# Optimization experiments

Hardware: AMD Instinct MI355X
Metric: run time of the kernel (lower is better)

Reference implementation:

```python
import jax, jax.numpy as jnp
import numpy as np

HEADS = 8
DIM_HEAD = 64
SPARSITY = 0.1  # sparsity_target * min(1, step_count/1000) with step_count >= 1000


def setup_inputs() -> dict:
    key = jax.random.key(0)
    k1, k2, k3, k4, k5 = jax.random.split(key, 5)
    b, n, d = 4, 2048, 512
    inner = HEADS * DIM_HEAD  # 512
    x = jax.random.normal(k1, (b, n, d), dtype=jnp.float32)
    # grad_ema buffer: EMA of squared attention gradients -> positive values
    grad_ema = jax.random.uniform(k2, (b, HEADS, n, n), dtype=jnp.float32)
    w_qkv = jax.random.normal(k3, (d, 3 * inner), dtype=jnp.float32) * 0.02
    w_out = jax.random.normal(k4, (inner, d), dtype=jnp.float32) * 0.02
    b_out = jax.random.normal(k5, (d,), dtype=jnp.float32) * 0.02
    return {"x": x, "grad_ema": grad_ema, "w_qkv": w_qkv, "w_out": w_out, "b_out": b_out}


def reference(x, grad_ema, w_qkv, w_out, b_out):
    b, n, d = x.shape
    h, dh = HEADS, DIM_HEAD
    scale = dh ** (-0.5)
    # QKV projection (no bias)
    qkv = x @ w_qkv  # [b, n, 3*h*dh]
    q, k, v = jnp.split(qkv, 3, axis=-1)
    def heads(t):  # [b, n, h*dh] -> [b, h, n, dh]
        return t.reshape(b, n, h, dh).transpose(0, 2, 1, 3)
    q, k, v = heads(q), heads(k), heads(v)
    dots = jnp.einsum("bhid,bhjd->bhij", q, k) * scale  # [b, h, n, n]
    # gradient-sculpted sparsity mask: keep entries with grad_ema above global quantile
    threshold = jnp.quantile(grad_ema, 1.0 - SPARSITY)
    dots = jnp.where(grad_ema >= threshold, dots, -jnp.inf)
    attn = jax.nn.softmax(dots, axis=-1)
    out = jnp.einsum("bhij,bhjd->bhid", attn, v)  # [b, h, n, dh]
    out = out.transpose(0, 2, 1, 3).reshape(b, n, h * dh)
    return out @ w_out + b_out
```

## Files before the change

kernel.cpp:

```cpp
#include <hip/hip_runtime.h>

typedef unsigned short u16;
typedef unsigned long long ull;
typedef __attribute__((ext_vector_type(8))) short bf16x8;
typedef __attribute__((ext_vector_type(4))) float f32x4;

#define LOG2E 1.44269504088896340736f

#define GN 134217728LL
#define LO_BITS 0x3F65FD8Bu
#define HI_BITS 0x3F66CF41u
#define NBINS (HI_BITS - LO_BITS)
#define SCAN_CHUNK 1024
#define NCHUNK ((int)((NBINS + SCAN_CHUNK - 1) / SCAN_CHUNK))

__device__ inline u16 f2bf(float f) {
    unsigned int u = __float_as_uint(f);
    unsigned int r = 0x7FFFu + ((u >> 16) & 1u);
    return (u16)((u + r) >> 16);
}

extern "C" __global__ __launch_bounds__(256)
void zero_k(unsigned int* __restrict__ hist, ull* __restrict__ hi_cnt) {
    int i = blockIdx.x * 256 + threadIdx.x;
    for (int b = i; b < (int)NBINS; b += 65536) hist[b] = 0u;
    if (i == 0) *hi_cnt = 0ull;
}

extern "C" __global__ __launch_bounds__(256)
void hist_k(const float* __restrict__ g, unsigned int* __restrict__ hist,
            ull* __restrict__ hi_cnt) {
    long long tid = (long long)blockIdx.x * 256 + threadIdx.x;
    long long stride = (long long)gridDim.x * 256;
    unsigned int hi = 0;
    const float4* g4 = (const float4*)g;
    const long long n4 = GN / 4;
    for (long long i = tid; i < n4; i += stride) {
        float4 v = g4[i];
        float vv[4] = {v.x, v.y, v.z, v.w};
#pragma unroll
        for (int c = 0; c < 4; ++c) {
            unsigned int u = __float_as_uint(vv[c]);
            if (u >= HI_BITS) hi++;
            else if (u >= LO_BITS) atomicAdd(&hist[u - LO_BITS], 1u);
        }
    }
#pragma unroll
    for (int off = 32; off; off >>= 1) hi += __shfl_down(hi, off, 64);
    if ((threadIdx.x & 63) == 0 && hi) atomicAdd(hi_cnt, (ull)hi);
}

extern "C" __global__ __launch_bounds__(256)
void scan_a(const unsigned int* __restrict__ hist, ull* __restrict__ csum) {
    __shared__ unsigned int part[256];
    int c = blockIdx.x;
    unsigned int s = 0;
    int base = c * SCAN_CHUNK;
    for (int i = threadIdx.x; i < SCAN_CHUNK; i += 256) {
        int b = base + i;
        if (b < (int)NBINS) s += hist[b];
    }
    part[threadIdx.x] = s;
    __syncthreads();
    for (int st = 128; st; st >>= 1) {
        if ((int)threadIdx.x < st) part[threadIdx.x] += part[threadIdx.x + st];
        __syncthreads();
    }
    if (threadIdx.x == 0) csum[c] = part[0];
}

extern "C" __global__ __launch_bounds__(256)
void scan_b(const unsigned int* __restrict__ hist, const ull* __restrict__ csum,
            const ull* __restrict__ hi_cnt, float* __restrict__ thr_out) {
    __shared__ ull cs[NCHUNK];
    __shared__ ull pre[NCHUNK];
    __shared__ ull cfine_s;
    __shared__ unsigned int wtot[4];
    __shared__ int ch_s;
    __shared__ ull chpre_s;
    __shared__ float vals_s[2];
    const int t = threadIdx.x;
    if (t < NCHUNK) cs[t] = csum[t];
    __syncthreads();
    if (t < NCHUNK) {
        ull s = 0;
        for (int j = 0; j < t; ++j) s += cs[j];
        pre[t] = s;
    }
    if (t == 0) {
        ull s = 0;
        for (int j = 0; j < NCHUNK; ++j) s += cs[j];
        cfine_s = s;
    }
    __syncthreads();
    const long long cfine = (long long)cfine_s;
    const long long chi = (long long)(*hi_cnt);
    const long long cbelow = GN - chi - cfine;
    const double h = 0.9 * (double)(GN - 1);
    const long long k = (long long)h;
    const double gfrac = h - (double)k;
    const long long tg0 = k - cbelow;

    for (int ti = 0; ti < 2; ++ti) {
        long long tgt = tg0 + ti;
        if (tgt < 0) { if (t == 0) vals_s[ti] = __uint_as_float(LO_BITS); __syncthreads(); continue; }
        if (tgt >= cfine) { if (t == 0) vals_s[ti] = __uint_as_float(HI_BITS); __syncthreads(); continue; }
        if (t < NCHUNK) {
            ull p = pre[t];
            if ((ull)tgt >= p && (ull)tgt < p + cs[t]) { ch_s = t; chpre_s = p; }
        }
        __syncthreads();
        const int base = ch_s * SCAN_CHUNK;
        const long long rel = tgt - (long long)chpre_s;
        unsigned int h4[4], s4 = 0;
#pragma unroll
        for (int q = 0; q < 4; ++q) {
            int b = base + t * 4 + q;
            unsigned int v = (b < (int)NBINS) ? hist[b] : 0u;
            h4[q] = v; s4 += v;
        }
        unsigned int sc = s4;
#pragma unroll
        for (int off = 1; off < 64; off <<= 1) {
            unsigned int y = __shfl_up(sc, off, 64);
            if ((t & 63) >= off) sc += y;
        }
        if ((t & 63) == 63) wtot[t >> 6] = sc;
        __syncthreads();
        unsigned int wbase = 0;
        for (int wv = 0; wv < (t >> 6); ++wv) wbase += wtot[wv];
        unsigned int incl = sc + wbase;
        unsigned int excl = incl - s4;
        if (rel >= (long long)excl && rel < (long long)incl) {
            long long rr = rel - excl;
            long long c2 = 0;
            int bsel = 3;
#pragma unroll
            for (int q = 0; q < 4; ++q) {
                if (c2 + (long long)h4[q] > rr) { bsel = q; break; }
                c2 += h4[q];
            }
            vals_s[ti] = __uint_as_float(LO_BITS + (unsigned int)(base + t * 4 + bsel));
        }
        __syncthreads();
    }
    if (t == 0) {
        double tv = (double)vals_s[0] + gfrac * ((double)vals_s[1] - (double)vals_s[0]);
        float tf = (float)tv;
        if ((double)tf < tv) tf = __uint_as_float(__float_as_uint(tf) + 1u);
        *thr_out = tf;
    }
}

extern "C" __global__ __launch_bounds__(256)
void conv_wt2(const float* __restrict__ wqkv, const float* __restrict__ wout,
              u16* __restrict__ wqt, u16* __restrict__ wot) {
    int bid = blockIdx.x;
    const float* w; u16* wt; int N; int id;
    if (bid < 3072) { w = wqkv; wt = wqt; N = 1536; id = bid * 256 + threadIdx.x; }
    else { w = wout; wt = wot; N = 512; id = (bid - 3072) * 256 + threadIdx.x; }
    int c = id / 512, k = id % 512;
    wt[id] = f2bf(w[(size_t)k * N + c]);
}

template <int MODE>
__global__ __launch_bounds__(256)
void gemm_bt(const float* __restrict__ Af, const u16* __restrict__ Ab, const u16* __restrict__ Bt,
             int M, int N, int K,
             u16* __restrict__ Qo, u16* __restrict__ Ko, u16* __restrict__ Vt,
             float* __restrict__ Cout, const float* __restrict__ bias) {
    __shared__ __align__(16) u16 As[128][64];
    __shared__ __align__(16) u16 Bs[128][64];
    const int t = threadIdx.x, w = t >> 6, l = t & 63;
    const int bm = blockIdx.x * 128, bn = blockIdx.y * 128;
    const int wm = (w >> 1) * 64, wn = (w & 1) * 64;
    const int lr = l & 15, lg = l >> 4;
    f32x4 acc[4][4] = {};
    for (int k0 = 0; k0 < K; k0 += 64) {
#pragma unroll
        for (int it = 0; it < 4; ++it) {
            int idx = it * 256 + t;
            int row = idx >> 3, ch = idx & 7;
            if constexpr (MODE == 0) {
                const float4* ap = (const float4*)&Af[(size_t)(bm + row) * K + k0 + ch * 8];
                float4 a0 = ap[0], a1 = ap[1];
                u16 tmp[8] = {f2bf(a0.x), f2bf(a0.y), f2bf(a0.z), f2bf(a0.w),
                              f2bf(a1.x), f2bf(a1.y), f2bf(a1.z), f2bf(a1.w)};
                *(bf16x8*)&As[row][(ch ^ (row & 7)) * 8] = *(bf16x8*)tmp;
            } else {
                *(bf16x8*)&As[row][(ch ^ (row & 7)) * 8] =
                    *(const bf16x8*)&Ab[(size_t)(bm + row) * K + k0 + ch * 8];
            }
        }
#pragma unroll
        for (int it = 0; it < 4; ++it) {
            int idx = it * 256 + t;
            int row = idx >> 3, ch = idx & 7;
            *(bf16x8*)&Bs[row][(ch ^ (row & 7)) * 8] =
                *(const bf16x8*)&Bt[(size_t)(bn + row) * K + k0 + ch * 8];
        }
        __syncthreads();
#pragma unroll
        for (int ks = 0; ks < 2; ++ks) {
            bf16x8 af[4], bfr[4];
#pragma unroll
            for (int i = 0; i < 4; ++i) {
                int row = wm + i * 16 + lr;
                int ci = ks * 4 + lg;
                af[i] = *(const bf16x8*)&As[row][(ci ^ (row & 7)) * 8];
            }
#pragma unroll
            for (int j = 0; j < 4; ++j) {
                int row = wn + j * 16 + lr;
                int ci = ks * 4 + lg;
                bfr[j] = *(const bf16x8*)&Bs[row][(ci ^ (row & 7)) * 8];
            }
#pragma unroll
            for (int i = 0; i < 4; ++i)
#pragma unroll
                for (int j = 0; j < 4; ++j)
                    acc[i][j] = __builtin_amdgcn_mfma_f32_16x16x32_bf16(af[i], bfr[j], acc[i][j], 0, 0, 0);
        }
        __syncthreads();
    }
#pragma unroll
    for (int i = 0; i < 4; ++i) {
#pragma unroll
        for (int j = 0; j < 4; ++j) {
            int col = bn + wn + j * 16 + lr;
#pragma unroll
            for (int r = 0; r < 4; ++r) {
                int row = bm + wm + i * 16 + lg * 4 + r;
                float v = acc[i][j][r];
                if constexpr (MODE == 0) {
                    int t3 = col >> 9;
                    int hh = (col >> 6) & 7;
                    int d = col & 63;
                    int b = row >> 11;
                    int tok = row & 2047;
                    int bh = b * 8 + hh;
                    if (t3 == 0) Qo[((size_t)bh * 2048 + tok) * 64 + d] = f2bf(v * 0.125f);
                    else if (t3 == 1) Ko[((size_t)bh * 2048 + tok) * 64 + d] = f2bf(v);
                    else Vt[((size_t)bh * 64 + d) * 2048 + tok] = f2bf(v);
                } else {
                    Cout[(size_t)row * N + col] = v + bias[col];
                }
            }
        }
    }
}

extern "C" __global__ __launch_bounds__(256)
void flash_k(const u16* __restrict__ Qb, const u16* __restrict__ Kb, const u16* __restrict__ Vt,
             const float* __restrict__ gema, const float* __restrict__ thrp,
             u16* __restrict__ HO) {
    __shared__ __align__(16) u16 Ks[64][64];
    __shared__ __align__(16) u16 Vs[64][64];
    __shared__ __align__(16) u16 Ps[4][32][64];
    const int t = threadIdx.x, w = t >> 6, l = t & 63;
    const int lr = l & 15, lg = l >> 4;
    const int bh = blockIdx.y;
    const int i0 = blockIdx.x * 128 + w * 32;
    const float thr = thrp[0];

    bf16x8 qf[2][2];
#pragma unroll
    for (int i2 = 0; i2 < 2; ++i2)
#pragma unroll
        for (int ks = 0; ks < 2; ++ks)
            qf[i2][ks] = *(const bf16x8*)&Qb[((size_t)bh * 2048 + i0 + i2 * 16 + lr) * 64 + ks * 32 + lg * 8];

    f32x4 o[2][4] = {};
    float mrow[2][4], lrow[2][4];
#pragma unroll
    for (int i2 = 0; i2 < 2; ++i2)
#pragma unroll
        for (int r = 0; r < 4; ++r) { mrow[i2][r] = -1e30f; lrow[i2][r] = 0.f; }

    const size_t gbase = (size_t)bh * 2048 * 2048;

    for (int jt = 0; jt < 2048; jt += 64) {
#pragma unroll
        for (int it = 0; it < 2; ++it) {
            int idx = it * 256 + t;
            int row = idx >> 3, ch = idx & 7;
            *(bf16x8*)&Ks[row][(ch ^ (row & 7)) * 8] =
                *(const bf16x8*)&Kb[((size_t)bh * 2048 + jt + row) * 64 + ch * 8];
            *(bf16x8*)&Vs[row][(ch ^ (row & 7)) * 8] =
                *(const bf16x8*)&Vt[((size_t)bh * 64 + row) * 2048 + jt + ch * 8];
        }
        __syncthreads();

        f32x4 sc[2][4] = {};
#pragma unroll
        for (int ks = 0; ks < 2; ++ks) {
#pragma unroll
            for (int jf = 0; jf < 4; ++jf) {
                int row = jf * 16 + lr;
                int ci = ks * 4 + lg;
                bf16x8 kf = *(const bf16x8*)&Ks[row][(ci ^ (row & 7)) * 8];
#pragma unroll
                for (int i2 = 0; i2 < 2; ++i2)
                    sc[i2][jf] = __builtin_amdgcn_mfma_f32_16x16x32_bf16(qf[i2][ks], kf, sc[i2][jf], 0, 0, 0);
            }
        }

        float tmax[2][4];
#pragma unroll
        for (int i2 = 0; i2 < 2; ++i2)
#pragma unroll
            for (int r = 0; r < 4; ++r) tmax[i2][r] = -1e30f;
#pragma unroll
        for (int i2 = 0; i2 < 2; ++i2) {
#pragma unroll
            for (int jf = 0; jf < 4; ++jf) {
                int j = jt + jf * 16 + lr;
#pragma unroll
                for (int r = 0; r < 4; ++r) {
                    int i = i0 + i2 * 16 + lg * 4 + r;
                    float g = gema[gbase + (size_t)i * 2048 + j];
                    float sv = sc[i2][jf][r];
                    sv = (g >= thr) ? sv : -1e30f;
                    sc[i2][jf][r] = sv;
                    tmax[i2][r] = fmaxf(tmax[i2][r], sv);
                }
            }
        }
#pragma unroll
        for (int i2 = 0; i2 < 2; ++i2)
#pragma unroll
            for (int r = 0; r < 4; ++r) {
                float m = tmax[i2][r];
                m = fmaxf(m, __shfl_xor(m, 1, 64));
                m = fmaxf(m, __shfl_xor(m, 2, 64));
                m = fmaxf(m, __shfl_xor(m, 4, 64));
                m = fmaxf(m, __shfl_xor(m, 8, 64));
                tmax[i2][r] = m;
            }

        float psum[2][4] = {};
#pragma unroll
        for (int i2 = 0; i2 < 2; ++i2) {
            bool need = false;
#pragma unroll
            for (int r = 0; r < 4; ++r) need |= (tmax[i2][r] > mrow[i2][r]);
            if (__any(need)) {
#pragma unroll
                for (int r = 0; r < 4; ++r) {
                    float mn = fmaxf(mrow[i2][r], tmax[i2][r]);
                    float alpha = exp2f((mrow[i2][r] - mn) * LOG2E);
                    mrow[i2][r] = mn;
                    lrow[i2][r] *= alpha;
#pragma unroll
                    for (int df = 0; df < 4; ++df) o[i2][df][r] *= alpha;
                }
            }
#pragma unroll
            for (int jf = 0; jf < 4; ++jf) {
#pragma unroll
                for (int r = 0; r < 4; ++r) {
                    float sv = sc[i2][jf][r];
                    float p = (sv > -1e29f) ? exp2f((sv - mrow[i2][r]) * LOG2E) : 0.f;
                    psum[i2][r] += p;
                    int prow = i2 * 16 + lg * 4 + r;
                    int colj = jf * 16 + lr;
                    int chv = colj >> 3, off = colj & 7;
                    Ps[w][prow][((chv ^ (prow & 7)) * 8) + off] = f2bf(p);
                }
            }
        }
#pragma unroll
        for (int i2 = 0; i2 < 2; ++i2)
#pragma unroll
            for (int r = 0; r < 4; ++r) {
                float ssum = psum[i2][r];
                ssum += __shfl_xor(ssum, 1, 64);
                ssum += __shfl_xor(ssum, 2, 64);
                ssum += __shfl_xor(ssum, 4, 64);
                ssum += __shfl_xor(ssum, 8, 64);
                lrow[i2][r] += ssum;
            }

#pragma unroll
        for (int i2 = 0; i2 < 2; ++i2) {
            bf16x8 pa[2];
#pragma unroll
            for (int js = 0; js < 2; ++js) {
                int prow = i2 * 16 + lr;
                int ci = js * 4 + lg;
                pa[js] = *(const bf16x8*)&Ps[w][prow][(ci ^ (prow & 7)) * 8];
            }
#pragma unroll
            for (int df = 0; df < 4; ++df) {
#pragma unroll
                for (int js = 0; js < 2; ++js) {
                    int vrow = df * 16 + lr;
                    int ci = js * 4 + lg;
                    bf16x8 vf = *(const bf16x8*)&Vs[vrow][(ci ^ (vrow & 7)) * 8];
                    o[i2][df] = __builtin_amdgcn_mfma_f32_16x16x32_bf16(pa[js], vf, o[i2][df], 0, 0, 0);
                }
            }
        }
        __syncthreads();
    }

    const int b = bh >> 3, hh = bh & 7;
#pragma unroll
    for (int i2 = 0; i2 < 2; ++i2) {
#pragma unroll
        for (int df = 0; df < 4; ++df) {
            int d = df * 16 + lr;
#pragma unroll
            for (int r = 0; r < 4; ++r) {
                int i = i0 + i2 * 16 + lg * 4 + r;
                float val = o[i2][df][r] / lrow[i2][r];
                HO[((size_t)(b * 2048 + i)) * 512 + hh * 64 + d] = f2bf(val);
            }
        }
    }
}

extern "C" void kernel_launch(void* const* d_in, const int* in_sizes, int n_in,
                              void* d_out, int out_size, void* d_ws, size_t ws_size,
                              hipStream_t stream) {
    const float* x = (const float*)d_in[0];
    const float* gema = (const float*)d_in[1];
    const float* wqkv = (const float*)d_in[2];
    const float* wout = (const float*)d_in[3];
    const float* bout = (const float*)d_in[4];
    float* out = (float*)d_out;
    char* ws = (char*)d_ws;

    const size_t HIST_OFF = 0;
    const size_t HI_OFF = 262144;
    const size_t THR_OFF = 262400;
    const size_t CSUM_OFF = 263168;
    const size_t Q_OFF = 524288;
    const size_t K_OFF = Q_OFF + 8388608;
    const size_t V_OFF = K_OFF + 8388608;
    const size_t SH_OFF = V_OFF + 8388608;
    const size_t WOT_OFF = SH_OFF + 8388608;
    const size_t NEED = WOT_OFF + 524288;
    if (ws_size < NEED) return;

    unsigned int* hist = (unsigned int*)(ws + HIST_OFF);
    ull* hi_cnt = (ull*)(ws + HI_OFF);
    float* thr = (float*)(ws + THR_OFF);
    ull* csum = (ull*)(ws + CSUM_OFF);
    u16* Q = (u16*)(ws + Q_OFF);
    u16* Kb = (u16*)(ws + K_OFF);
    u16* Vt = (u16*)(ws + V_OFF);
    u16* wqt = (u16*)(ws + SH_OFF);
    u16* HO = (u16*)(ws + SH_OFF);
    u16* wot = (u16*)(ws + WOT_OFF);

    zero_k<<<256, 256, 0, stream>>>(hist, hi_cnt);
    conv_wt2<<<4096, 256, 0, stream>>>(wqkv, wout, wqt, wot);
    gemm_bt<0><<<dim3(64, 12), 256, 0, stream>>>(x, nullptr, wqt, 8192, 1536, 512,
                                                 Q, Kb, Vt, nullptr, nullptr);
    hist_k<<<2048, 256, 0, stream>>>(gema, hist, hi_cnt);
    scan_a<<<NCHUNK, 256, 0, stream>>>(hist, csum);
    scan_b<<<1, 256, 0, stream>>>(hist, csum, hi_cnt, thr);
    flash_k<<<dim3(16, 32), 256, 0, stream>>>(Q, Kb, Vt, gema, thr, HO);
    gemm_bt<1><<<dim3(64, 4), 256, 0, stream>>>(nullptr, HO, wot, 8192, 512, 512,
                                                nullptr, nullptr, nullptr, out, bout);
}
```

Baseline: 435.5 us.

## Co-schedule QKV GEMM with histogram pass and halve flash-attention row tile

Merges the QKV projection GEMM and the grad_ema histogram pass into one launch, with separate block ranges doing each job, so the memory-bound histogram can overlap the compute-bound GEMM and one launch is removed. The flash attention kernel now gives each wave 16 query rows instead of 32 and launches twice as many blocks (32x32 grid), which raises parallelism and lowers register pressure. The cost is that every K/V tile is loaded into shared memory twice as often per query row, and the mixed-role fused kernel must reserve GEMM shared memory even in histogram blocks.

```diff
diff --git a/kernel.cpp b/kernel.cpp
--- a/kernel.cpp
+++ b/kernel.cpp
@@ -13,6 +13,8 @@
 #define NBINS (HI_BITS - LO_BITS)
 #define SCAN_CHUNK 1024
 #define NCHUNK ((int)((NBINS + SCAN_CHUNK - 1) / SCAN_CHUNK))
+#define GEMM0_BLKS 768
+#define HIST_BLKS 2048
 
 __device__ inline u16 f2bf(float f) {
     unsigned int u = __float_as_uint(f);
@@ -28,26 +30,113 @@
 }
 
 extern "C" __global__ __launch_bounds__(256)
-void hist_k(const float* __restrict__ g, unsigned int* __restrict__ hist,
-            ull* __restrict__ hi_cnt) {
-    long long tid = (long long)blockIdx.x * 256 + threadIdx.x;
-    long long stride = (long long)gridDim.x * 256;
-    unsigned int hi = 0;
-    const float4* g4 = (const float4*)g;
-    const long long n4 = GN / 4;
-    for (long long i = tid; i < n4; i += stride) {
-        float4 v = g4[i];
-        float vv[4] = {v.x, v.y, v.z, v.w};
-#pragma unroll
-        for (int c = 0; c < 4; ++c) {
-            unsigned int u = __float_as_uint(vv[c]);
-            if (u >= HI_BITS) hi++;
-            else if (u >= LO_BITS) atomicAdd(&hist[u - LO_BITS], 1u);
-        }
-    }
-#pragma unroll
-    for (int off = 32; off; off >>= 1) hi += __shfl_down(hi, off, 64);
-    if ((threadIdx.x & 63) == 0 && hi) atomicAdd(hi_cnt, (ull)hi);
+void conv_wt2(const float* __restrict__ wqkv, const float* __restrict__ wout,
+              u16* __restrict__ wqt, u16* __restrict__ wot) {
+    int bid = blockIdx.x;
+    const float* w; u16* wt; int N; int id;
+    if (bid < 3072) { w = wqkv; wt = wqt; N = 1536; id = bid * 256 + threadIdx.x; }
+    else { w = wout; wt = wot; N = 512; id = (bid - 3072) * 256 + threadIdx.x; }
+    int c = id / 512, k = id % 512;
+    wt[id] = f2bf(w[(size_t)k * N + c]);
+}
+
+extern "C" __global__ __launch_bounds__(256)
+void fused0_k(const float* __restrict__ Af, const u16* __restrict__ Bt,
+              u16* __restrict__ Qo, u16* __restrict__ Ko, u16* __restrict__ Vt,
+              const float* __restrict__ g, unsigned int* __restrict__ hist,
+              ull* __restrict__ hi_cnt) {
+    if (blockIdx.x >= GEMM0_BLKS) {
+        long long tid = (long long)(blockIdx.x - GEMM0_BLKS) * 256 + threadIdx.x;
+        const long long stride = (long long)HIST_BLKS * 256;
+        unsigned int hi = 0;
+        const float4* g4 = (const float4*)g;
+        const long long n4 = GN / 4;
+        for (long long i = tid; i < n4; i += stride) {
+            float4 v = g4[i];
+            float vv[4] = {v.x, v.y, v.z, v.w};
+#pragma unroll
+            for (int c = 0; c < 4; ++c) {
+                unsigned int u = __float_as_uint(vv[c]);
+                if (u >= HI_BITS) hi++;
+                else if (u >= LO_BITS) atomicAdd(&hist[u - LO_BITS], 1u);
+            }
+        }
+#pragma unroll
+        for (int off = 32; off; off >>= 1) hi += __shfl_down(hi, off, 64);
+        if ((threadIdx.x & 63) == 0 && hi) atomicAdd(hi_cnt, (ull)hi);
+        return;
+    }
+    __shared__ __align__(16) u16 As[128][64];
+    __shared__ __align__(16) u16 Bs[128][64];
+    const int t = threadIdx.x, w = t >> 6, l = t & 63;
+    const int bm = (blockIdx.x & 63) * 128, bn = (blockIdx.x >> 6) * 128;
+    const int wm = (w >> 1) * 64, wn = (w & 1) * 64;
+    const int lr = l & 15, lg = l >> 4;
+    const int K = 512;
+    f32x4 acc[4][4] = {};
+    for (int k0 = 0; k0 < K; k0 += 64) {
+#pragma unroll
+        for (int it = 0; it < 4; ++it) {
+            int idx = it * 256 + t;
+            int row = idx >> 3, ch = idx & 7;
+            const float4* ap = (const float4*)&Af[(size_t)(bm + row) * K + k0 + ch * 8];
+            float4 a0 = ap[0], a1 = ap[1];
+            u16 tmp[8] = {f2bf(a0.x), f2bf(a0.y), f2bf(a0.z), f2bf(a0.w),
+                          f2bf(a1.x), f2bf(a1.y), f2bf(a1.z), f2bf(a1.w)};
+            *(bf16x8*)&As[row][(ch ^ (row & 7)) * 8] = *(bf16x8*)tmp;
+        }
+#pragma unroll
+        for (int it = 0; it < 4; ++it) {
+            int idx = it * 256 + t;
+            int row = idx >> 3, ch = idx & 7;
+            *(bf16x8*)&Bs[row][(ch ^ (row & 7)) * 8] =
+                *(const bf16x8*)&Bt[(size_t)(bn + row) * K + k0 + ch * 8];
+        }
+        __syncthreads();
+#pragma unroll
+        for (int ks = 0; ks < 2; ++ks) {
+            bf16x8 af[4], bfr[4];
+#pragma unroll
+            for (int i = 0; i < 4; ++i) {
+                int row = wm + i * 16 + lr;
+                int ci = ks * 4 + lg;
+                af[i] = *(const bf16x8*)&As[row][(ci ^ (row & 7)) * 8];
+            }
+#pragma unroll
+            for (int j = 0; j < 4; ++j) {
+                int row = wn + j * 16 + lr;
+                int ci = ks * 4 + lg;
+                bfr[j] = *(const bf16x8*)&Bs[row][(ci ^ (row & 7)) * 8];
+            }
+#pragma unroll
+            for (int i = 0; i < 4; ++i)
+#pragma unroll
+                for (int j = 0; j < 4; ++j)
+                    acc[i][j] = __builtin_amdgcn_mfma_f32_16x16x32_bf16(af[i], bfr[j], acc[i][j], 0, 0, 0);
+        }
+        __syncthreads();
+    }
+#pragma unroll
+    for (int i = 0; i < 4; ++i) {
+#pragma unroll
+        for (int j = 0; j < 4; ++j) {
+            int col = bn + wn + j * 16 + lr;
+            int t3 = col >> 9;
+            int hh = (col >> 6) & 7;
+            int d = col & 63;
+#pragma unroll
+            for (int r = 0; r < 4; ++r) {
+                int row = bm + wm + i * 16 + lg * 4 + r;
+                int b = row >> 11;
+                int tok = row & 2047;
+                int bh = b * 8 + hh;
+                float v = acc[i][j][r];
+                if (t3 == 0) Qo[((size_t)bh * 2048 + tok) * 64 + d] = f2bf(v * 0.125f);
+                else if (t3 == 1) Ko[((size_t)bh * 2048 + tok) * 64 + d] = f2bf(v);
+                else Vt[((size_t)bh * 64 + d) * 2048 + tok] = f2bf(v);
+            }
+        }
+    }
 }
 
 extern "C" __global__ __launch_bounds__(256)
@@ -152,23 +241,9 @@
     }
 }
 
-extern "C" __global__ __launch_bounds__(256)
-void conv_wt2(const float* __restrict__ wqkv, const float* __restrict__ wout,
-              u16* __restrict__ wqt, u16* __restrict__ wot) {
-    int bid = blockIdx.x;
-    const float* w; u16* wt; int N; int id;
-    if (bid < 3072) { w = wqkv; wt = wqt; N = 1536; id = bid * 256 + threadIdx.x; }
-    else { w = wout; wt = wot; N = 512; id = (bid - 3072) * 256 + threadIdx.x; }
-    int c = id / 512, k = id % 512;
-    wt[id] = f2bf(w[(size_t)k * N + c]);
-}
-
-template <int MODE>
 __global__ __launch_bounds__(256)
-void gemm_bt(const float* __restrict__ Af, const u16* __restrict__ Ab, const u16* __restrict__ Bt,
-             int M, int N, int K,
-             u16* __restrict__ Qo, u16* __restrict__ Ko, u16* __restrict__ Vt,
-             float* __restrict__ Cout, const float* __restrict__ bias) {
+void gemm_out(const u16* __restrict__ Ab, const u16* __restrict__ Bt,
+              int M, int N, int K, float* __restrict__ Cout, const float* __restrict__ bias) {
     __shared__ __align__(16) u16 As[128][64];
     __shared__ __align__(16) u16 Bs[128][64];
     const int t = threadIdx.x, w = t >> 6, l = t & 63;
@@ -181,16 +256,8 @@
         for (int it = 0; it < 4; ++it) {
             int idx = it * 256 + t;
             int row = idx >> 3, ch = idx & 7;
-            if constexpr (MODE == 0) {
-                const float4* ap = (const float4*)&Af[(size_t)(bm + row) * K + k0 + ch * 8];
-                float4 a0 = ap[0], a1 = ap[1];
-                u16 tmp[8] = {f2bf(a0.x), f2bf(a0.y), f2bf(a0.z), f2bf(a0.w),
-                              f2bf(a1.x), f2bf(a1.y), f2bf(a1.z), f2bf(a1.w)};
-                *(bf16x8*)&As[row][(ch ^ (row & 7)) * 8] = *(bf16x8*)tmp;
-            } else {
-                *(bf16x8*)&As[row][(ch ^ (row & 7)) * 8] =
-                    *(const bf16x8*)&Ab[(size_t)(bm + row) * K + k0 + ch * 8];
-            }
+            *(bf16x8*)&As[row][(ch ^ (row & 7)) * 8] =
+                *(const bf16x8*)&Ab[(size_t)(bm + row) * K + k0 + ch * 8];
         }
 #pragma unroll
         for (int it = 0; it < 4; ++it) {
@@ -224,30 +291,16 @@
         __syncthreads();
     }
 #pragma unroll
-    for (int i = 0; i < 4; ++i) {
+    for (int i = 0; i < 4; ++i)
 #pragma unroll
         for (int j = 0; j < 4; ++j) {
             int col = bn + wn + j * 16 + lr;
 #pragma unroll
             for (int r = 0; r < 4; ++r) {
                 int row = bm + wm + i * 16 + lg * 4 + r;
-                float v = acc[i][j][r];
-                if constexpr (MODE == 0) {
-                    int t3 = col >> 9;
-                    int hh = (col >> 6) & 7;
-                    int d = col & 63;
-                    int b = row >> 11;
-                    int tok = row & 2047;
-                    int bh = b * 8 + hh;
-                    if (t3 == 0) Qo[((size_t)bh * 2048 + tok) * 64 + d] = f2bf(v * 0.125f);
-                    else if (t3 == 1) Ko[((size_t)bh * 2048 + tok) * 64 + d] = f2bf(v);
-                    else Vt[((size_t)bh * 64 + d) * 2048 + tok] = f2bf(v);
-                } else {
-                    Cout[(size_t)row * N + col] = v + bias[col];
-                }
-            }
-        }
-    }
+                Cout[(size_t)row * N + col] = acc[i][j][r] + bias[col];
+            }
+        }
 }
 
 extern "C" __global__ __launch_bounds__(256)
@@ -256,26 +309,22 @@
              u16* __restrict__ HO) {
     __shared__ __align__(16) u16 Ks[64][64];
     __shared__ __align__(16) u16 Vs[64][64];
-    __shared__ __align__(16) u16 Ps[4][32][64];
+    __shared__ __align__(16) u16 Ps[4][16][64];
     const int t = threadIdx.x, w = t >> 6, l = t & 63;
     const int lr = l & 15, lg = l >> 4;
     const int bh = blockIdx.y;
-    const int i0 = blockIdx.x * 128 + w * 32;
+    const int i0 = blockIdx.x * 64 + w * 16;
     const float thr = thrp[0];
 
-    bf16x8 qf[2][2];
-#pragma unroll
-    for (int i2 = 0; i2 < 2; ++i2)
-#pragma unroll
-        for (int ks = 0; ks < 2; ++ks)
-            qf[i2][ks] = *(const bf16x8*)&Qb[((size_t)bh * 2048 + i0 + i2 * 16 + lr) * 64 + ks * 32 + lg * 8];
-
-    f32x4 o[2][4] = {};
-    float mrow[2][4], lrow[2][4];
-#pragma unroll
-    for (int i2 = 0; i2 < 2; ++i2)
-#pragma unroll
-        for (int r = 0; r < 4; ++r) { mrow[i2][r] = -1e30f; lrow[i2][r] = 0.f; }
+    bf16x8 qf[2];
+#pragma unroll
+    for (int ks = 0; ks < 2; ++ks)
+        qf[ks] = *(const bf16x8*)&Qb[((size_t)bh * 2048 + i0 + lr) * 64 + ks * 32 + lg * 8];
+
+    f32x4 o[4] = {};
+    float mrow[4], lrow[4];
+#pragma unroll
+    for (int r = 0; r < 4; ++r) { mrow[r] = -1e30f; lrow[r] = 0.f; }
 
     const size_t gbase = (size_t)bh * 2048 * 2048;
 
@@ -291,7 +340,7 @@
         }
         __syncthreads();
 
-        f32x4 sc[2][4] = {};
+        f32x4 sc[4] = {};
 #pragma unroll
         for (int ks = 0; ks < 2; ++ks) {
 #pragma unroll
@@ -299,106 +348,86 @@
                 int row = jf * 16 + lr;
                 int ci = ks * 4 + lg;
                 bf16x8 kf = *(const bf16x8*)&Ks[row][(ci ^ (row & 7)) * 8];
-#pragma unroll
-                for (int i2 = 0; i2 < 2; ++i2)
-                    sc[i2][jf] = __builtin_amdgcn_mfma_f32_16x16x32_bf16(qf[i2][ks], kf, sc[i2][jf], 0, 0, 0);
-            }
-        }
-
-        float tmax[2][4];
-#pragma unroll
-        for (int i2 = 0; i2 < 2; ++i2)
-#pragma unroll
-            for (int r = 0; r < 4; ++r) tmax[i2][r] = -1e30f;
-#pragma unroll
-        for (int i2 = 0; i2 < 2; ++i2) {
-#pragma unroll
-            for (int jf = 0; jf < 4; ++jf) {
-                int j = jt + jf * 16 + lr;
-#pragma unroll
-                for (int r = 0; r < 4; ++r) {
-                    int i = i0 + i2 * 16 + lg * 4 + r;
-                    float g = gema[gbase + (size_t)i * 2048 + j];
-                    float sv = sc[i2][jf][r];
-                    sv = (g >= thr) ? sv : -1e30f;
-                    sc[i2][jf][r] = sv;
-                    tmax[i2][r] = fmaxf(tmax[i2][r], sv);
-                }
-            }
-        }
-#pragma unroll
-        for (int i2 = 0; i2 < 2; ++i2)
+                sc[jf] = __builtin_amdgcn_mfma_f32_16x16x32_bf16(qf[ks], kf, sc[jf], 0, 0, 0);
+            }
+        }
+
+        float tmax[4] = {-1e30f, -1e30f, -1e30f, -1e30f};
+#pragma unroll
+        for (int jf = 0; jf < 4; ++jf) {
+            int j = jt + jf * 16 + lr;
 #pragma unroll
             for (int r = 0; r < 4; ++r) {
-                float m = tmax[i2][r];
-                m = fmaxf(m, __shfl_xor(m, 1, 64));
-                m = fmaxf(m, __shfl_xor(m, 2, 64));
-                m = fmaxf(m, __shfl_xor(m, 4, 64));
-                m = fmaxf(m, __shfl_xor(m, 8, 64));
-                tmax[i2][r] = m;
-            }
-
-        float psum[2][4] = {};
-#pragma unroll
-        for (int i2 = 0; i2 < 2; ++i2) {
-            bool need = false;
-#pragma unroll
-            for (int r = 0; r < 4; ++r) need |= (tmax[i2][r] > mrow[i2][r]);
-            if (__any(need)) {
-#pragma unroll
-                for (int r = 0; r < 4; ++r) {
-                    float mn = fmaxf(mrow[i2][r], tmax[i2][r]);
-                    float alpha = exp2f((mrow[i2][r] - mn) * LOG2E);
-                    mrow[i2][r] = mn;
-                    lrow[i2][r] *= alpha;
-#pragma unroll
-                    for (int df = 0; df < 4; ++df) o[i2][df][r] *= alpha;
-                }
-            }
-#pragma unroll
-            for (int jf = 0; jf < 4; ++jf) {
-#pragma unroll
-                for (int r = 0; r < 4; ++r) {
-                    float sv = sc[i2][jf][r];
-                    float p = (sv > -1e29f) ? exp2f((sv - mrow[i2][r]) * LOG2E) : 0.f;
-                    psum[i2][r] += p;
-                    int prow = i2 * 16 + lg * 4 + r;
-                    int colj = jf * 16 + lr;
-                    int chv = colj >> 3, off = colj & 7;
-                    Ps[w][prow][((chv ^ (prow & 7)) * 8) + off] = f2bf(p);
-                }
-            }
-        }
-#pragma unroll
-        for (int i2 = 0; i2 < 2; ++i2)
+                int i = i0 + lg * 4 + r;
+                float g = gema[gbase + (size_t)i * 2048 + j];
+                float sv = sc[jf][r];
+                sv = (g >= thr) ? sv : -1e30f;
+                sc[jf][r] = sv;
+                tmax[r] = fmaxf(tmax[r], sv);
+            }
+        }
+#pragma unroll
+        for (int r = 0; r < 4; ++r) {
+            float m = tmax[r];
+            m = fmaxf(m, __shfl_xor(m, 1, 64));
+            m = fmaxf(m, __shfl_xor(m, 2, 64));
+            m = fmaxf(m, __shfl_xor(m, 4, 64));
+            m = fmaxf(m, __shfl_xor(m, 8, 64));
+            tmax[r] = m;
+        }
+
+        bool need = false;
+#pragma unroll
+        for (int r = 0; r < 4; ++r) need |= (tmax[r] > mrow[r]);
+        if (__any(need)) {
 #pragma unroll
             for (int r = 0; r < 4; ++r) {
-                float ssum = psum[i2][r];
-                ssum += __shfl_xor(ssum, 1, 64);
-                ssum += __shfl_xor(ssum, 2, 64);
-                ssum += __shfl_xor(ssum, 4, 64);
-                ssum += __shfl_xor(ssum, 8, 64);
-                lrow[i2][r] += ssum;
-            }
-
-#pragma unroll
-        for (int i2 = 0; i2 < 2; ++i2) {
-            bf16x8 pa[2];
+                float mn = fmaxf(mrow[r], tmax[r]);
+                float alpha = exp2f((mrow[r] - mn) * LOG2E);
+                mrow[r] = mn;
+                lrow[r] *= alpha;
+#pragma unroll
+                for (int df = 0; df < 4; ++df) o[df][r] *= alpha;
+            }
+        }
+        float psum[4] = {};
+#pragma unroll
+        for (int jf = 0; jf < 4; ++jf) {
+#pragma unroll
+            for (int r = 0; r < 4; ++r) {
+                float sv = sc[jf][r];
+                float p = (sv > -1e29f) ? exp2f((sv - mrow[r]) * LOG2E) : 0.f;
+                psum[r] += p;
+                int prow = lg * 4 + r;
+                int colj = jf * 16 + lr;
+                int chv = colj >> 3, off = colj & 7;
+                Ps[w][prow][((chv ^ (prow & 7)) * 8) + off] = f2bf(p);
+            }
+        }
+#pragma unroll
+        for (int r = 0; r < 4; ++r) {
+            float ssum = psum[r];
+            ssum += __shfl_xor(ssum, 1, 64);
+            ssum += __shfl_xor(ssum, 2, 64);
+            ssum += __shfl_xor(ssum, 4, 64);
+            ssum += __shfl_xor(ssum, 8, 64);
+            lrow[r] += ssum;
+        }
+
+        bf16x8 pa[2];
+#pragma unroll
+        for (int js = 0; js < 2; ++js) {
+            int ci = js * 4 + lg;
+            pa[js] = *(const bf16x8*)&Ps[w][lr][(ci ^ (lr & 7)) * 8];
+        }
+#pragma unroll
+        for (int df = 0; df < 4; ++df) {
 #pragma unroll
             for (int js = 0; js < 2; ++js) {
-                int prow = i2 * 16 + lr;
+                int vrow = df * 16 + lr;
                 int ci = js * 4 + lg;
-                pa[js] = *(const bf16x8*)&Ps[w][prow][(ci ^ (prow & 7)) * 8];
-            }
-#pragma unroll
-            for (int df = 0; df < 4; ++df) {
-#pragma unroll
-                for (int js = 0; js < 2; ++js) {
-                    int vrow = df * 16 + lr;
-                    int ci = js * 4 + lg;
-                    bf16x8 vf = *(const bf16x8*)&Vs[vrow][(ci ^ (vrow & 7)) * 8];
-                    o[i2][df] = __builtin_amdgcn_mfma_f32_16x16x32_bf16(pa[js], vf, o[i2][df], 0, 0, 0);
-                }
+                bf16x8 vf = *(const bf16x8*)&Vs[vrow][(ci ^ (vrow & 7)) * 8];
+                o[df] = __builtin_amdgcn_mfma_f32_16x16x32_bf16(pa[js], vf, o[df], 0, 0, 0);
             }
         }
         __syncthreads();
@@ -406,16 +435,13 @@
 
     const int b = bh >> 3, hh = bh & 7;
 #pragma unroll
-    for (int i2 = 0; i2 < 2; ++i2) {
-#pragma unroll
-        for (int df = 0; df < 4; ++df) {
-            int d = df * 16 + lr;
-#pragma unroll
-            for (int r = 0; r < 4; ++r) {
-                int i = i0 + i2 * 16 + lg * 4 + r;
-                float val = o[i2][df][r] / lrow[i2][r];
-                HO[((size_t)(b * 2048 + i)) * 512 + hh * 64 + d] = f2bf(val);
-            }
+    for (int df = 0; df < 4; ++df) {
+        int d = df * 16 + lr;
+#pragma unroll
+        for (int r = 0; r < 4; ++r) {
+            int i = i0 + lg * 4 + r;
+            float val = o[df][r] / lrow[r];
+            HO[((size_t)(b * 2048 + i)) * 512 + hh * 64 + d] = f2bf(val);
         }
     }
 }
@@ -456,12 +482,10 @@
 
     zero_k<<<256, 256, 0, stream>>>(hist, hi_cnt);
     conv_wt2<<<4096, 256, 0, stream>>>(wqkv, wout, wqt, wot);
-    gemm_bt<0><<<dim3(64, 12), 256, 0, stream>>>(x, nullptr, wqt, 8192, 1536, 512,
-                                                 Q, Kb, Vt, nullptr, nullptr);
-    hist_k<<<2048, 256, 0, stream>>>(gema, hist, hi_cnt);
+    fused0_k<<<GEMM0_BLKS + HIST_BLKS, 256, 0, stream>>>(x, wqt, Q, Kb, Vt,
+                                                         gema, hist, hi_cnt);
     scan_a<<<NCHUNK, 256, 0, stream>>>(hist, csum);
     scan_b<<<1, 256, 0, stream>>>(hist, csum, hi_cnt, thr);
-    flash_k<<<dim3(16, 32), 256, 0, stream>>>(Q, Kb, Vt, gema, thr, HO);
-    gemm_bt<1><<<dim3(64, 4), 256, 0, stream>>>(nullptr, HO, wot, 8192, 512, 512,
-                                                nullptr, nullptr, nullptr, out, bout);
-}
+    flash_k<<<dim3(32, 32), 256, 0, stream>>>(Q, Kb, Vt, gema, thr, HO);
+    gemm_out<<<dim3(64, 4), 256, 0, stream>>>(HO, wot, 8192, 512, 512, out, bout);
+}
```

After: 540.9 us. 1.24x slower.

## Split flash attention over key dimension and merge partial results

Applied to the files above, without the earlier changes.

Splits the attention kernel's key loop into two halves across a new grid dimension, doubling the block count from 512 to 1024. Each half writes unnormalized fp32 partial outputs plus its row max and sum, and a new combine kernel merges them with rescaling before writing bf16 head outputs. The goal is better occupancy across the many compute units, at the cost of an extra kernel launch and roughly 34 MB of extra fp32 traffic to workspace.

```diff
diff --git a/kernel.cpp b/kernel.cpp
--- a/kernel.cpp
+++ b/kernel.cpp
@@ -13,6 +13,7 @@
 #define NBINS (HI_BITS - LO_BITS)
 #define SCAN_CHUNK 1024
 #define NCHUNK ((int)((NBINS + SCAN_CHUNK - 1) / SCAN_CHUNK))
+#define NROWS 65536
 
 __device__ inline u16 f2bf(float f) {
     unsigned int u = __float_as_uint(f);
@@ -253,13 +254,14 @@
 extern "C" __global__ __launch_bounds__(256)
 void flash_k(const u16* __restrict__ Qb, const u16* __restrict__ Kb, const u16* __restrict__ Vt,
              const float* __restrict__ gema, const float* __restrict__ thrp,
-             u16* __restrict__ HO) {
+             float* __restrict__ op, float2* __restrict__ ml) {
     __shared__ __align__(16) u16 Ks[64][64];
     __shared__ __align__(16) u16 Vs[64][64];
     __shared__ __align__(16) u16 Ps[4][32][64];
     const int t = threadIdx.x, w = t >> 6, l = t & 63;
     const int lr = l & 15, lg = l >> 4;
     const int bh = blockIdx.y;
+    const int js = blockIdx.z;
     const int i0 = blockIdx.x * 128 + w * 32;
     const float thr = thrp[0];
 
@@ -278,8 +280,9 @@
         for (int r = 0; r < 4; ++r) { mrow[i2][r] = -1e30f; lrow[i2][r] = 0.f; }
 
     const size_t gbase = (size_t)bh * 2048 * 2048;
-
-    for (int jt = 0; jt < 2048; jt += 64) {
+    const int jlo = js * 1024, jhi = jlo + 1024;
+
+    for (int jt = jlo; jt < jhi; jt += 64) {
 #pragma unroll
         for (int it = 0; it < 2; ++it) {
             int idx = it * 256 + t;
@@ -385,39 +388,59 @@
         for (int i2 = 0; i2 < 2; ++i2) {
             bf16x8 pa[2];
 #pragma unroll
-            for (int js = 0; js < 2; ++js) {
+            for (int js2 = 0; js2 < 2; ++js2) {
                 int prow = i2 * 16 + lr;
-                int ci = js * 4 + lg;
-                pa[js] = *(const bf16x8*)&Ps[w][prow][(ci ^ (prow & 7)) * 8];
+                int ci = js2 * 4 + lg;
+                pa[js2] = *(const bf16x8*)&Ps[w][prow][(ci ^ (prow & 7)) * 8];
             }
 #pragma unroll
             for (int df = 0; df < 4; ++df) {
 #pragma unroll
-                for (int js = 0; js < 2; ++js) {
+                for (int js2 = 0; js2 < 2; ++js2) {
                     int vrow = df * 16 + lr;
-                    int ci = js * 4 + lg;
+                    int ci = js2 * 4 + lg;
                     bf16x8 vf = *(const bf16x8*)&Vs[vrow][(ci ^ (vrow & 7)) * 8];
-                    o[i2][df] = __builtin_amdgcn_mfma_f32_16x16x32_bf16(pa[js], vf, o[i2][df], 0, 0, 0);
+                    o[i2][df] = __builtin_amdgcn_mfma_f32_16x16x32_bf16(pa[js2], vf, o[i2][df], 0, 0, 0);
                 }
             }
         }
         __syncthreads();
     }
 
-    const int b = bh >> 3, hh = bh & 7;
+    const size_t rbase = (size_t)(js * 32 + bh) * 2048;
 #pragma unroll
     for (int i2 = 0; i2 < 2; ++i2) {
 #pragma unroll
-        for (int df = 0; df < 4; ++df) {
-            int d = df * 16 + lr;
-#pragma unroll
-            for (int r = 0; r < 4; ++r) {
-                int i = i0 + i2 * 16 + lg * 4 + r;
-                float val = o[i2][df][r] / lrow[i2][r];
-                HO[((size_t)(b * 2048 + i)) * 512 + hh * 64 + d] = f2bf(val);
-            }
-        }
-    }
+        for (int r = 0; r < 4; ++r) {
+            int i = i0 + i2 * 16 + lg * 4 + r;
+#pragma unroll
+            for (int df = 0; df < 4; ++df)
+                op[(rbase + i) * 64 + df * 16 + lr] = o[i2][df][r];
+            if (lr == 0) ml[rbase + i] = make_float2(mrow[i2][r], lrow[i2][r]);
+        }
+    }
+}
+
+extern "C" __global__ __launch_bounds__(256)
+void combine_k(const float* __restrict__ op, const float2* __restrict__ ml,
+               u16* __restrict__ HO) {
+    int row = blockIdx.x * 8 + (threadIdx.x >> 5);
+    int d2 = threadIdx.x & 31;
+    float2 ml0 = ml[row];
+    float2 ml1 = ml[NROWS + row];
+    float m = fmaxf(ml0.x, ml1.x);
+    float a0 = exp2f((ml0.x - m) * LOG2E);
+    float a1 = exp2f((ml1.x - m) * LOG2E);
+    float linv = 1.0f / (ml0.y * a0 + ml1.y * a1);
+    const float2* o2 = (const float2*)op;
+    float2 v0 = o2[(size_t)row * 32 + d2];
+    float2 v1 = o2[((size_t)NROWS + row) * 32 + d2];
+    float r0 = (v0.x * a0 + v1.x * a1) * linv;
+    float r1 = (v0.y * a0 + v1.y * a1) * linv;
+    int bh = row >> 11, i = row & 2047, b = bh >> 3, hh = bh & 7;
+    u16 pair[2] = {f2bf(r0), f2bf(r1)};
+    *(unsigned int*)&HO[((size_t)(b * 2048 + i)) * 512 + hh * 64 + d2 * 2] =
+        *(unsigned int*)pair;
 }
 
 extern "C" void kernel_launch(void* const* d_in, const int* in_sizes, int n_in,
@@ -440,7 +463,9 @@
     const size_t V_OFF = K_OFF + 8388608;
     const size_t SH_OFF = V_OFF + 8388608;
     const size_t WOT_OFF = SH_OFF + 8388608;
-    const size_t NEED = WOT_OFF + 524288;
+    const size_t OP_OFF = WOT_OFF + 524288;
+    const size_t ML_OFF = OP_OFF + 33554432;
+    const size_t NEED = ML_OFF + 1048576;
     if (ws_size < NEED) return;
 
     unsigned int* hist = (unsigned int*)(ws + HIST_OFF);
@@ -453,6 +478,8 @@
     u16* wqt = (u16*)(ws + SH_OFF);
     u16* HO = (u16*)(ws + SH_OFF);
     u16* wot = (u16*)(ws + WOT_OFF);
+    float* op = (float*)(ws + OP_OFF);
+    float2* ml = (float2*)(ws + ML_OFF);
 
     zero_k<<<256, 256, 0, stream>>>(hist, hi_cnt);
     conv_wt2<<<4096, 256, 0, stream>>>(wqkv, wout, wqt, wot);
@@ -461,7 +488,8 @@
     hist_k<<<2048, 256, 0, stream>>>(gema, hist, hi_cnt);
     scan_a<<<NCHUNK, 256, 0, stream>>>(hist, csum);
     scan_b<<<1, 256, 0, stream>>>(hist, csum, hi_cnt, thr);
-    flash_k<<<dim3(16, 32), 256, 0, stream>>>(Q, Kb, Vt, gema, thr, HO);
+    flash_k<<<dim3(16, 32, 2), 256, 0, stream>>>(Q, Kb, Vt, gema, thr, op, ml);
+    combine_k<<<8192, 256, 0, stream>>>(op, ml, HO);
     gemm_bt<1><<<dim3(64, 4), 256, 0, stream>>>(nullptr, HO, wot, 8192, 512, 512,
                                                 nullptr, nullptr, nullptr, out, bout);
 }
```

Measured after the change: 583.6 us. +34.0%, slower.

## Prefetch grad_ema mask tiles into LDS via async global_load_lds double-step

Applied to the files above, without the earlier changes.

Replaces the per-element strided global reads of grad_ema in the flash kernel with asynchronous global_load_lds copies of the next 32x64 tile per wave into a 32KB LDS buffer. The load for tile jt+64 is issued after the current tile's mask is applied, so the dominant 512MB grad_ema stream overlaps with MFMA and softmax work. Barriers become explicit lgkmcnt waits plus s_barrier, and a vmcnt(0) wait precedes the mask reads. The extra LDS may reduce occupancy.

```diff
diff --git a/kernel.cpp b/kernel.cpp
--- a/kernel.cpp
+++ b/kernel.cpp
@@ -257,11 +257,16 @@
     __shared__ __align__(16) u16 Ks[64][64];
     __shared__ __align__(16) u16 Vs[64][64];
     __shared__ __align__(16) u16 Ps[4][32][64];
+    __shared__ __align__(16) float G[8192];
     const int t = threadIdx.x, w = t >> 6, l = t & 63;
     const int lr = l & 15, lg = l >> 4;
     const int bh = blockIdx.y;
-    const int i0 = blockIdx.x * 128 + w * 32;
+    const int ib = blockIdx.x * 128;
+    const int i0 = ib + w * 32;
     const float thr = thrp[0];
+
+    typedef const __attribute__((address_space(1))) unsigned int gu32;
+    typedef __attribute__((address_space(3))) unsigned int lu32;
 
     bf16x8 qf[2][2];
 #pragma unroll
@@ -278,6 +283,25 @@
         for (int r = 0; r < 4; ++r) { mrow[i2][r] = -1e30f; lrow[i2][r] = 0.f; }
 
     const size_t gbase = (size_t)bh * 2048 * 2048;
+    const float* grow0 = &gema[gbase + (size_t)(ib + w * 32 + (l >> 4)) * 2048 + (l & 15) * 4];
+
+#define ISSUE_G(JT)                                                                   \
+    do {                                                                              \
+        _Pragma("unroll")                                                             \
+        for (int c2 = 0; c2 < 8; ++c2) {                                              \
+            const float* gp = grow0 + (size_t)(c2 * 4) * 2048 + (JT);                 \
+            __builtin_amdgcn_global_load_lds((gu32*)gp, (lu32*)&G[(w * 8 + c2) * 256],\
+                                             16, 0, 0);                               \
+        }                                                                             \
+    } while (0)
+
+#define BAR_LGKM()                                                     \
+    do {                                                               \
+        asm volatile("s_waitcnt lgkmcnt(0)" ::: "memory");             \
+        __builtin_amdgcn_s_barrier();                                  \
+    } while (0)
+
+    ISSUE_G(0);
 
     for (int jt = 0; jt < 2048; jt += 64) {
 #pragma unroll
@@ -289,7 +313,7 @@
             *(bf16x8*)&Vs[row][(ch ^ (row & 7)) * 8] =
                 *(const bf16x8*)&Vt[((size_t)bh * 64 + row) * 2048 + jt + ch * 8];
         }
-        __syncthreads();
+        BAR_LGKM();
 
         f32x4 sc[2][4] = {};
 #pragma unroll
@@ -305,6 +329,9 @@
             }
         }
 
+        asm volatile("s_waitcnt vmcnt(0)" ::: "memory");
+        __builtin_amdgcn_sched_barrier(0);
+
         float tmax[2][4];
 #pragma unroll
         for (int i2 = 0; i2 < 2; ++i2)
@@ -313,19 +340,20 @@
 #pragma unroll
         for (int i2 = 0; i2 < 2; ++i2) {
 #pragma unroll
-            for (int jf = 0; jf < 4; ++jf) {
-                int j = jt + jf * 16 + lr;
-#pragma unroll
-                for (int r = 0; r < 4; ++r) {
-                    int i = i0 + i2 * 16 + lg * 4 + r;
-                    float g = gema[gbase + (size_t)i * 2048 + j];
+            for (int r = 0; r < 4; ++r) {
+                int rowb = (w * 32 + i2 * 16 + lg * 4 + r) * 64;
+#pragma unroll
+                for (int jf = 0; jf < 4; ++jf) {
                     float sv = sc[i2][jf][r];
-                    sv = (g >= thr) ? sv : -1e30f;
+                    sv = (G[rowb + jf * 16 + lr] >= thr) ? sv : -1e30f;
                     sc[i2][jf][r] = sv;
                     tmax[i2][r] = fmaxf(tmax[i2][r], sv);
                 }
             }
         }
+
+        if (jt < 2048 - 64) ISSUE_G(jt + 64);
+
 #pragma unroll
         for (int i2 = 0; i2 < 2; ++i2)
 #pragma unroll
@@ -401,8 +429,10 @@
                 }
             }
         }
-        __syncthreads();
-    }
+        BAR_LGKM();
+    }
+#undef ISSUE_G
+#undef BAR_LGKM
 
     const int b = bh >> 3, hh = bh & 7;
 #pragma unroll
```

After: 538.8 us. 1.24x slower.
